# Kernel tuning notes

Hardware: AMD Instinct MI355X
Metric: run time of the kernel (lower is better)

The kernel has to match this reference:

```python
import jax, jax.numpy as jnp
import numpy as np

D_MODEL = 1024
D_FFN = 4096
NUM_EXPERTS = 8
TOP_K = 2
EPS = 1e-7


def setup_inputs() -> dict:
    key = jax.random.key(0)
    ks = jax.random.split(key, 10)
    B, T = 2, 2048
    s = 0.02
    return {
        "x": jax.random.normal(ks[0], (B, T, D_MODEL), dtype=jnp.float32),
        "padding_mask": jnp.ones((B, T), dtype=bool),
        "rms_w": jnp.ones((D_MODEL,), dtype=jnp.float32),
        "router_w": jax.random.normal(ks[1], (NUM_EXPERTS, D_MODEL), dtype=jnp.float32) * s,
        "router_b": jnp.zeros((NUM_EXPERTS,), dtype=jnp.float32),
        "W1": jax.random.normal(ks[2], (NUM_EXPERTS, D_MODEL, D_FFN), dtype=jnp.float32) * s,
        "b1": jnp.zeros((NUM_EXPERTS, D_FFN), dtype=jnp.float32),
        "W2": jax.random.normal(ks[3], (NUM_EXPERTS, D_FFN, D_MODEL), dtype=jnp.float32) * s,
        "b2": jnp.zeros((NUM_EXPERTS, D_MODEL), dtype=jnp.float32),
        "W3": jax.random.normal(ks[4], (NUM_EXPERTS, D_MODEL, D_FFN), dtype=jnp.float32) * s,
        "b3": jnp.zeros((NUM_EXPERTS, D_FFN), dtype=jnp.float32),
    }


def reference(x, padding_mask, rms_w, router_w, router_b, W1, b1, W2, b2, W3, b3):
    B, T, d = x.shape
    # RMSNorm
    rms = jnp.sqrt(jnp.mean(x * x, axis=-1, keepdims=True) + EPS)
    xn = rms_w * (x / rms)
    xf = xn.reshape(-1, d)  # [N, d]

    # Router: softmax -> top-k -> renormalize
    logits = xf @ router_w.T + router_b            # [N, E]
    probs = jax.nn.softmax(logits, axis=-1)
    topv, topi = jax.lax.top_k(probs, TOP_K)       # [N, K]
    w = topv / jnp.sum(topv, axis=-1, keepdims=True)
    # Dense combine weights per (token, expert): sum of top-k weights routed to e
    combine = jnp.sum(jax.nn.one_hot(topi, NUM_EXPERTS, dtype=xf.dtype) * w[..., None], axis=1)  # [N, E]

    # Loop over experts via scan (one full-token SwiGLU FFN per expert, masked combine)
    def step(acc, params):
        W1e, b1e, W2e, b2e, W3e, b3e, ce = params
        h = jax.nn.silu(xf @ W1e + b1e) * (xf @ W3e + b3e)  # [N, d_ffn]
        y = h @ W2e + b2e                                    # [N, d]
        return acc + ce[:, None] * y, None

    out, _ = jax.lax.scan(step, jnp.zeros_like(xf), (W1, b1, W2, b2, W3, b3, combine.T))
    aux_loss = jnp.asarray(0.0, dtype=x.dtype)  # use_aux_loss only active in training mode
    return out.reshape(B, T, d), aux_loss
```

## Files before the change

kernel.cpp:

```cpp
#include <hip/hip_runtime.h>
#include <stdint.h>


#define NTOK 4096
#define DM   1024
#define DF   4096
#define NE   8
#define BM   128
#define MAX_RB 72
#define SLOT_CAP (MAX_RB * BM)

typedef _Float16 f16;
typedef __attribute__((ext_vector_type(8))) _Float16 f16x8;
typedef __attribute__((ext_vector_type(4))) _Float16 f16x4;
typedef __attribute__((ext_vector_type(4))) float    f32x4;
typedef __attribute__((ext_vector_type(2))) float    f32x2;

__device__ __forceinline__ void gl2lds16(const void* g, void* l) {
  __builtin_amdgcn_global_load_lds(
      (const __attribute__((address_space(1))) unsigned int*)g,
      (__attribute__((address_space(3))) unsigned int*)l, 16, 0, 0);
}

__global__ __launch_bounds__(256) void k_rms_router(
    const float* __restrict__ x, const float* __restrict__ rms_w,
    const float* __restrict__ rw, const float* __restrict__ rbias,
    f16* __restrict__ xn, int* __restrict__ topi, float* __restrict__ topw,
    int* __restrict__ counts)
{
  int t = blockIdx.x;
  int tid = threadIdx.x;
  const float* xr = x + (size_t)t * DM;
  f32x4 xv = *(const f32x4*)(xr + tid * 4);
  f32x4 gw = *(const f32x4*)(rms_w + tid * 4);
  f32x4 gv = xv * gw;

  float v[9];
  v[8] = xv[0]*xv[0] + xv[1]*xv[1] + xv[2]*xv[2] + xv[3]*xv[3];
#pragma unroll
  for (int e = 0; e < NE; ++e) {
    f32x4 wv = *(const f32x4*)(rw + e * DM + tid * 4);
    v[e] = gv[0]*wv[0] + gv[1]*wv[1] + gv[2]*wv[2] + gv[3]*wv[3];
  }
#pragma unroll
  for (int off = 32; off; off >>= 1) {
#pragma unroll
    for (int j = 0; j < 9; ++j) v[j] += __shfl_xor(v[j], off);
  }
  __shared__ float red[4][9];
  int wave = tid >> 6, lane = tid & 63;
  if (lane == 0) {
#pragma unroll
    for (int j = 0; j < 9; ++j) red[wave][j] = v[j];
  }
  __syncthreads();
  float tot[9];
#pragma unroll
  for (int j = 0; j < 9; ++j)
    tot[j] = red[0][j] + red[1][j] + red[2][j] + red[3][j];

  float rinv = 1.0f / sqrtf(tot[8] * (1.0f / DM) + 1e-7f);
  float lg[NE];
#pragma unroll
  for (int e = 0; e < NE; ++e) lg[e] = tot[e] * rinv + rbias[e];

  int e1 = 0; float b1v = lg[0];
#pragma unroll
  for (int e = 1; e < NE; ++e) if (lg[e] > b1v) { b1v = lg[e]; e1 = e; }
  int e2 = -1; float b2v = -1e30f;
#pragma unroll
  for (int e = 0; e < NE; ++e) if (e != e1 && lg[e] > b2v) { b2v = lg[e]; e2 = e; }

  float r2 = expf(b2v - b1v);
  float w1 = 1.0f / (1.0f + r2);
  float w2 = r2 * w1;

  if (tid == 0) {
    topi[t * 2 + 0] = e1; topi[t * 2 + 1] = e2;
    topw[t * 2 + 0] = w1; topw[t * 2 + 1] = w2;
    atomicAdd(&counts[e1], 1);
    atomicAdd(&counts[e2], 1);
  }
  f16x4 o;
#pragma unroll
  for (int i = 0; i < 4; ++i) o[i] = (f16)(gv[i] * rinv);
  *(f16x4*)(xn + (size_t)t * DM + tid * 4) = o;
}

__global__ void k_build(const int* __restrict__ counts, int* __restrict__ po,
                        int2* __restrict__ rbtable, int* __restrict__ total_rb)
{
  if (threadIdx.x != 0 || blockIdx.x != 0) return;
  int off = 0, idx = 0;
  for (int e = 0; e < NE; ++e) {
    int c = counts[e];
    po[e] = off;
    int nrb = (c + BM - 1) / BM;
    for (int r = 0; r < nrb; ++r) { rbtable[idx] = make_int2(e, off + r * BM); ++idx; }
    off += nrb * BM;
  }
  *total_rb = idx;
}

__global__ __launch_bounds__(256) void k_assign(
    const int* __restrict__ topi, const float* __restrict__ topw,
    const int* __restrict__ po, int* __restrict__ cursors,
    int* __restrict__ slot_token, float* __restrict__ slot_w,
    int* __restrict__ tok2slot)
{
  int t = blockIdx.x * 256 + threadIdx.x;
  if (t >= NTOK) return;
#pragma unroll
  for (int k = 0; k < 2; ++k) {
    int e = topi[t * 2 + k];
    int pos = atomicAdd(&cursors[e], 1);
    int slot = po[e] + pos;
    slot_token[slot] = t;
    slot_w[slot] = topw[t * 2 + k];
    tok2slot[t * 2 + k] = slot;
  }
}

__global__ __launch_bounds__(256) void k_convw(
    const float* __restrict__ W1, const float* __restrict__ W3,
    f16* __restrict__ w16)
{
  __shared__ f16 T[64][132];
  int g = blockIdx.x;
  int tensor = g >> 12;
  int rem = g & 4095;
  int e = rem >> 9;
  int t = rem & 511;
  const float* W = (tensor == 0) ? W1 : W3;
  int np = t >> 4, kt = t & 15;
  const float* src = W + (size_t)e * DM * DF + (size_t)(kt * 64) * DF + np * 128;

  int tid = threadIdx.x;
  int q = tid & 31, kb = tid >> 5;
#pragma unroll
  for (int i = 0; i < 8; ++i) {
    int k = kb + 8 * i;
    f32x4 v = *(const f32x4*)(src + (size_t)k * DF + q * 4);
    f16x4 h4 = { (f16)v[0], (f16)v[1], (f16)v[2], (f16)v[3] };
    *(f16x4*)(&T[k][q * 4]) = h4;
  }
  __syncthreads();
  int n = tid >> 1;
  f16* dst = w16 + ((size_t)(tensor * NE + e) * 512 + t) * 8192 + n * 64 + (tid & 1) * 32;
#pragma unroll
  for (int qq = 0; qq < 4; ++qq) {
    int cs = (tid & 1) * 4 + qq;
    int cl = cs ^ (n & 7);
    f16x8 o;
#pragma unroll
    for (int j = 0; j < 8; ++j) o[j] = T[cl * 8 + j][n];
    *(f16x8*)(dst + qq * 8) = o;
  }
}

__global__ __launch_bounds__(256, 3) void k_ffn13(
    const f16* __restrict__ xn, const int* __restrict__ slot_token,
    const int2* __restrict__ rbtable, const int* __restrict__ total_rb,
    const f16* __restrict__ w16,
    const float* __restrict__ b1, const float* __restrict__ b3,
    const float* __restrict__ W2, f16* __restrict__ w16_w2,
    f16* __restrict__ h)
{
  __shared__ __align__(16) f16 As[128 * 64];
  __shared__ __align__(16) f16 Bs[2][128 * 64];

  int bid = blockIdx.x;
  int wl = (bid & 7) * 288 + (bid >> 3);
  int rbi = wl % 72;
  int np  = wl / 72;
  int tid = threadIdx.x, lane = tid & 63, wave = tid >> 6;

  bool active = (rbi < *total_rb);
  if (active) {
    int2 ent = rbtable[rbi];
    int e = ent.x, row0 = ent.y;
    int n0 = np * 128;

    int wm = wave >> 1, wn = wave & 1;
    const f16* wb1 = w16 + ((size_t)(0 * NE + e) * 512 + np * 16) * 8192;
    const f16* wb3 = w16 + ((size_t)(1 * NE + e) * 512 + np * 16) * 8192;

    int tok[4];
#pragma unroll
    for (int q = 0; q < 4; ++q) {
      int m = q * 32 + wave * 8 + (lane >> 3);
      int tkn = slot_token[row0 + m];
      tok[q] = (tkn < 0) ? 0 : tkn;
    }
    int csx = (((lane & 7) ^ (lane >> 3)) << 3);
    int lin = wave * 512 + lane * 8;

    f32x4 acc1[4][4], acc3[4][4];
    f32x4 z = {0.f, 0.f, 0.f, 0.f};
#pragma unroll
    for (int i = 0; i < 4; ++i)
#pragma unroll
      for (int j = 0; j < 4; ++j) { acc1[i][j] = z; acc3[i][j] = z; }

    for (int kt = 0; kt < DM / 64; ++kt) {
      int k0 = kt * 64;
      const f16* s1 = wb1 + (size_t)kt * 8192;
      const f16* s3 = wb3 + (size_t)kt * 8192;
#pragma unroll
      for (int q = 0; q < 4; ++q) {
        gl2lds16(xn + (size_t)tok[q] * DM + k0 + csx,
                 (char*)As + q * 4096 + wave * 1024);
        gl2lds16(s1 + q * 2048 + lin, (char*)Bs[0] + q * 4096 + wave * 1024);
        gl2lds16(s3 + q * 2048 + lin, (char*)Bs[1] + q * 4096 + wave * 1024);
      }
      __syncthreads();
#pragma unroll
      for (int kh = 0; kh < 2; ++kh) {
        int kk = kh * 32 + (lane >> 4) * 8;
        f16x8 a[4];
#pragma unroll
        for (int fm = 0; fm < 4; ++fm) {
          int m = wm * 64 + fm * 16 + (lane & 15);
          a[fm] = *(const f16x8*)((char*)As + m * 128 + 2 * (kk ^ ((m & 7) << 3)));
        }
#pragma unroll
        for (int fn = 0; fn < 4; ++fn) {
          int n = wn * 64 + fn * 16 + (lane & 15);
          f16x8 bf1 = *(const f16x8*)((char*)Bs[0] + n * 128 + 2 * (kk ^ ((n & 7) << 3)));
          f16x8 bf3 = *(const f16x8*)((char*)Bs[1] + n * 128 + 2 * (kk ^ ((n & 7) << 3)));
#pragma unroll
          for (int fm = 0; fm < 4; ++fm) {
            acc1[fm][fn] = __builtin_amdgcn_mfma_f32_16x16x32_f16(a[fm], bf1, acc1[fm][fn], 0, 0, 0);
            acc3[fm][fn] = __builtin_amdgcn_mfma_f32_16x16x32_f16(a[fm], bf3, acc3[fm][fn], 0, 0, 0);
          }
        }
      }
      __syncthreads();
    }
#pragma unroll
    for (int fn = 0; fn < 4; ++fn) {
      int nc = n0 + wn * 64 + fn * 16 + (lane & 15);
      float bb1 = b1[e * DF + nc], bb3 = b3[e * DF + nc];
#pragma unroll
      for (int fm = 0; fm < 4; ++fm) {
        int mbase = wm * 64 + fm * 16 + (lane >> 4) * 4;
#pragma unroll
        for (int r = 0; r < 4; ++r) {
          int sl = mbase + r;
          float u1 = acc1[fm][fn][r] + bb1;
          float u3 = acc3[fm][fn][r] + bb3;
          float hv = (u1 / (1.0f + __expf(-u1))) * u3;
          size_t off = (size_t)(row0 + sl) * DF + (nc & ~63)
                     + ((((nc >> 3) & 7) ^ (sl & 7)) << 3) + (nc & 7);
          h[off] = (f16)hv;
        }
      }
    }
  }

  f16 (*T)[132] = (f16(*)[132])(&Bs[0][0]);
  int q = tid & 31, kb = tid >> 5;
  for (int j = 0; j < 2; ++j) {
    int tile = bid * 2 + j;
    if (tile >= NE * 512) break;
    int e2 = tile >> 9, t2 = tile & 511;
    int np2 = t2 >> 6, kt2 = t2 & 63;
    const float* src = W2 + (size_t)e2 * DM * DF + (size_t)(kt2 * 64) * DM + np2 * 128;
    __syncthreads();
#pragma unroll
    for (int i = 0; i < 8; ++i) {
      int k = kb + 8 * i;
      f32x4 v = *(const f32x4*)(src + (size_t)k * DM + q * 4);
      f16x4 h4 = { (f16)v[0], (f16)v[1], (f16)v[2], (f16)v[3] };
      *(f16x4*)(&T[k][q * 4]) = h4;
    }
    __syncthreads();
    int n = tid >> 1;
    f16* dst = w16_w2 + (size_t)(e2 * 512 + t2) * 8192 + n * 64 + (tid & 1) * 32;
#pragma unroll
    for (int qq = 0; qq < 4; ++qq) {
      int cs = (tid & 1) * 4 + qq;
      int cl = cs ^ (n & 7);
      f16x8 o8;
#pragma unroll
      for (int jj = 0; jj < 8; ++jj) o8[jj] = T[cl * 8 + jj][n];
      *(f16x8*)(dst + qq * 8) = o8;
    }
  }
}

__global__ __launch_bounds__(256, 4) void k_ffn2(
    const f16* __restrict__ h,
    const int2* __restrict__ rbtable, const int* __restrict__ total_rb,
    const f16* __restrict__ w16_w2, f16* __restrict__ partial)
{
  int bid = blockIdx.x;
  int wl = (bid & 7) * 144 + (bid >> 3);
  int rbi = wl % 72;
  int rest = wl / 72;
  int kc = rest & 1;
  int np = rest >> 1;
  if (rbi >= *total_rb) return;
  int2 ent = rbtable[rbi];
  int e = ent.x, row0 = ent.y;
  int n0 = np * 128;

  __shared__ __align__(16) f16 As[128 * 64];
  __shared__ __align__(16) f16 Bsh[128 * 64];

  int tid = threadIdx.x, lane = tid & 63, wave = tid >> 6;
  int wm = wave >> 1, wn = wave & 1;
  const f16* wb = w16_w2 + ((size_t)e * 512 + np * 64 + kc * 32) * 8192;
  int lin = wave * 512 + lane * 8;

  f32x4 acc[4][4];
  f32x4 z = {0.f, 0.f, 0.f, 0.f};
#pragma unroll
  for (int i = 0; i < 4; ++i)
#pragma unroll
    for (int j = 0; j < 4; ++j) acc[i][j] = z;

  for (int kt = 0; kt < 32; ++kt) {
    const f16* sB = wb + (size_t)kt * 8192;
    int k0 = kc * 2048 + kt * 64;
#pragma unroll
    for (int q = 0; q < 4; ++q) {
      int m = q * 32 + wave * 8 + (lane >> 3);
      gl2lds16(h + (size_t)(row0 + m) * DF + k0 + ((lane & 7) << 3),
               (char*)As + q * 4096 + wave * 1024);
      gl2lds16(sB + q * 2048 + lin, (char*)Bsh + q * 4096 + wave * 1024);
    }
    __syncthreads();
#pragma unroll
    for (int kh = 0; kh < 2; ++kh) {
      int kk = kh * 32 + (lane >> 4) * 8;
      f16x8 a[4];
#pragma unroll
      for (int fm = 0; fm < 4; ++fm) {
        int m = wm * 64 + fm * 16 + (lane & 15);
        a[fm] = *(const f16x8*)((char*)As + m * 128 + 2 * (kk ^ ((m & 7) << 3)));
      }
#pragma unroll
      for (int fn = 0; fn < 4; ++fn) {
        int n = wn * 64 + fn * 16 + (lane & 15);
        f16x8 bf = *(const f16x8*)((char*)Bsh + n * 128 + 2 * (kk ^ ((n & 7) << 3)));
#pragma unroll
        for (int fm = 0; fm < 4; ++fm)
          acc[fm][fn] = __builtin_amdgcn_mfma_f32_16x16x32_f16(a[fm], bf, acc[fm][fn], 0, 0, 0);
      }
    }
    __syncthreads();
  }
#pragma unroll
  for (int fn = 0; fn < 4; ++fn) {
    int nc = n0 + wn * 64 + fn * 16 + (lane & 15);
#pragma unroll
    for (int fm = 0; fm < 4; ++fm) {
      int mbase = wm * 64 + fm * 16 + (lane >> 4) * 4;
#pragma unroll
      for (int r = 0; r < 4; ++r) {
        int slot = row0 + mbase + r;
        partial[((size_t)(kc * SLOT_CAP + slot) << 10) + nc] = (f16)acc[fm][fn][r];
      }
    }
  }
}

__global__ __launch_bounds__(256) void k_combine(
    const f16* __restrict__ partial, const int* __restrict__ tok2slot,
    const int* __restrict__ topi, const float* __restrict__ topw,
    const float* __restrict__ b2, float* __restrict__ out)
{
  int t = blockIdx.x;
  int nc = threadIdx.x * 4;
  int s1 = tok2slot[t * 2], s2 = tok2slot[t * 2 + 1];
  float c1 = topw[t * 2], c2 = topw[t * 2 + 1];
  int e1 = topi[t * 2], e2 = topi[t * 2 + 1];
  float y1[4] = {0.f, 0.f, 0.f, 0.f}, y2[4] = {0.f, 0.f, 0.f, 0.f};
#pragma unroll
  for (int kc = 0; kc < 2; ++kc) {
    f16x4 p1 = *(const f16x4*)(partial + (((size_t)(kc * SLOT_CAP + s1)) << 10) + nc);
    f16x4 p2 = *(const f16x4*)(partial + (((size_t)(kc * SLOT_CAP + s2)) << 10) + nc);
#pragma unroll
    for (int i = 0; i < 4; ++i) { y1[i] += (float)p1[i]; y2[i] += (float)p2[i]; }
  }
  f32x4 bb1 = *(const f32x4*)(b2 + e1 * DM + nc);
  f32x4 bb2 = *(const f32x4*)(b2 + e2 * DM + nc);
  f32x4 o;
#pragma unroll
  for (int i = 0; i < 4; ++i)
    o[i] = c1 * (y1[i] + bb1[i]) + c2 * (y2[i] + bb2[i]);
  *(f32x4*)(out + ((size_t)t << 10) + nc) = o;
}

extern "C" void kernel_launch(void* const* d_in, const int* in_sizes, int n_in,
                              void* d_out, int out_size, void* d_ws, size_t ws_size,
                              hipStream_t stream)
{
  const float* x     = (const float*)d_in[0];
  const float* rms_w = (const float*)d_in[2];
  const float* rw    = (const float*)d_in[3];
  const float* rbias = (const float*)d_in[4];
  const float* W1    = (const float*)d_in[5];
  const float* b1    = (const float*)d_in[6];
  const float* W2    = (const float*)d_in[7];
  const float* b2    = (const float*)d_in[8];
  const float* W3    = (const float*)d_in[9];
  const float* b3    = (const float*)d_in[10];
  float* out = (float*)d_out;

  char* ws = (char*)d_ws;
  size_t o = 0;
  f16* w16 = (f16*)(ws + o); o += (size_t)3 * NE * 512 * 8192 * 2;
  f16* h   = (f16*)(ws + o); o += (size_t)SLOT_CAP * DF * 2;
  f16* xn  = (f16*)(ws + o); o += (size_t)NTOK * DM * 2;
  int*   slot_token = (int*)(ws + o);   o += SLOT_CAP * 4;
  float* slot_w     = (float*)(ws + o); o += SLOT_CAP * 4;
  int*   topi       = (int*)(ws + o);   o += NTOK * 2 * 4;
  float* topw       = (float*)(ws + o); o += NTOK * 2 * 4;
  int*   tok2slot   = (int*)(ws + o);   o += NTOK * 2 * 4;
  int*   counts     = (int*)(ws + o);   o += 64;
  int*   cursors    = (int*)(ws + o);   o += 64;
  int*   po         = (int*)(ws + o);   o += 64;
  int*   total_rb   = (int*)(ws + o);   o += 64;
  int2*  rbtable    = (int2*)(ws + o);  o += MAX_RB * 8;
  (void)ws_size; (void)in_sizes; (void)n_in;

  f16* w16_w2 = w16 + (size_t)2 * NE * 512 * 8192;

  f16* partial = w16;

  hipMemsetAsync(d_out, 0, (size_t)out_size * 4, stream);
  hipMemsetAsync(counts, 0, 128, stream);
  hipMemsetAsync(slot_token, 0xFF, SLOT_CAP * 4, stream);

  k_convw<<<2 * NE * 512, 256, 0, stream>>>(W1, W3, w16);
  k_rms_router<<<NTOK, 256, 0, stream>>>(x, rms_w, rw, rbias, xn, topi, topw, counts);
  k_build<<<1, 64, 0, stream>>>(counts, po, rbtable, total_rb);
  k_assign<<<16, 256, 0, stream>>>(topi, topw, po, cursors, slot_token, slot_w, tok2slot);
  k_ffn13<<<8 * 288, 256, 0, stream>>>(xn, slot_token, rbtable, total_rb,
                                       w16, b1, b3, W2, w16_w2, h);
  k_ffn2<<<8 * 144, 256, 0, stream>>>(h, rbtable, total_rb, w16_w2, partial);
  k_combine<<<NTOK, 256, 0, stream>>>(partial, tok2slot, topi, topw, b2, out);
}
```

Before: 536.3 us.

## Triple-buffer FFN GEMMs with 512-thread blocks and async LDS prefetch

Both FFN GEMM kernels now run with 512-thread blocks over one 144KB LDS buffer. K-tiles are staged three deep with global_load_lds, and the loop waits on vmcnt with a raw barrier instead of a full __syncthreads, so loads overlap MFMA work. s_setprio raises wave priority around the MFMA bursts. In k_ffn13, half the waves compute the W1 GEMM and half the W3 GEMM, and the W3 results pass through LDS for the SwiGLU epilogue. k_ffn2 now covers 256 output columns per block with a 4-way K split, which doubles the partial buffers that the combine kernel reads. Only one block fits per CU, and the 4-way split adds partial-sum traffic.

After: 592.1 us. +10.4%, slower.

```diff
diff --git a/kernel.cpp b/kernel.cpp
--- a/kernel.cpp
+++ b/kernel.cpp
@@ -14,7 +14,6 @@
 typedef __attribute__((ext_vector_type(8))) _Float16 f16x8;
 typedef __attribute__((ext_vector_type(4))) _Float16 f16x4;
 typedef __attribute__((ext_vector_type(4))) float    f32x4;
-typedef __attribute__((ext_vector_type(2))) float    f32x2;
 
 __device__ __forceinline__ void gl2lds16(const void* g, void* l) {
   __builtin_amdgcn_global_load_lds(
@@ -158,7 +157,7 @@
   }
 }
 
-__global__ __launch_bounds__(256, 3) void k_ffn13(
+__global__ __launch_bounds__(512, 2) void k_ffn13(
     const f16* __restrict__ xn, const int* __restrict__ slot_token,
     const int2* __restrict__ rbtable, const int* __restrict__ total_rb,
     const f16* __restrict__ w16,
@@ -166,8 +165,7 @@
     const float* __restrict__ W2, f16* __restrict__ w16_w2,
     f16* __restrict__ h)
 {
-  __shared__ __align__(16) f16 As[128 * 64];
-  __shared__ __align__(16) f16 Bs[2][128 * 64];
+  __shared__ __align__(16) char LB[147456];
 
   int bid = blockIdx.x;
   int wl = (bid & 7) * 288 + (bid >> 3);
@@ -180,106 +178,135 @@
     int2 ent = rbtable[rbi];
     int e = ent.x, row0 = ent.y;
     int n0 = np * 128;
-
-    int wm = wave >> 1, wn = wave & 1;
+    int wm = wave >> 2, wt = (wave >> 1) & 1, wn = wave & 1;
+
     const f16* wb1 = w16 + ((size_t)(0 * NE + e) * 512 + np * 16) * 8192;
     const f16* wb3 = w16 + ((size_t)(1 * NE + e) * 512 + np * 16) * 8192;
 
-    int tok[4];
-#pragma unroll
-    for (int q = 0; q < 4; ++q) {
-      int m = q * 32 + wave * 8 + (lane >> 3);
+    int tok[2];
+#pragma unroll
+    for (int q = 0; q < 2; ++q) {
+      int m = q * 64 + wave * 8 + (lane >> 3);
       int tkn = slot_token[row0 + m];
       tok[q] = (tkn < 0) ? 0 : tkn;
     }
     int csx = (((lane & 7) ^ (lane >> 3)) << 3);
     int lin = wave * 512 + lane * 8;
 
-    f32x4 acc1[4][4], acc3[4][4];
+    f32x4 acc[4][4];
     f32x4 z = {0.f, 0.f, 0.f, 0.f};
 #pragma unroll
     for (int i = 0; i < 4; ++i)
 #pragma unroll
-      for (int j = 0; j < 4; ++j) { acc1[i][j] = z; acc3[i][j] = z; }
-
-    for (int kt = 0; kt < DM / 64; ++kt) {
-      int k0 = kt * 64;
+      for (int j = 0; j < 4; ++j) acc[i][j] = z;
+
+    auto STAGE = [&](int kt, int ro) {
       const f16* s1 = wb1 + (size_t)kt * 8192;
       const f16* s3 = wb3 + (size_t)kt * 8192;
-#pragma unroll
-      for (int q = 0; q < 4; ++q) {
-        gl2lds16(xn + (size_t)tok[q] * DM + k0 + csx,
-                 (char*)As + q * 4096 + wave * 1024);
-        gl2lds16(s1 + q * 2048 + lin, (char*)Bs[0] + q * 4096 + wave * 1024);
-        gl2lds16(s3 + q * 2048 + lin, (char*)Bs[1] + q * 4096 + wave * 1024);
-      }
-      __syncthreads();
+      int k0 = kt * 64;
+#pragma unroll
+      for (int q = 0; q < 2; ++q) {
+        int d = ro + q * 8192 + wave * 1024 + lane * 16;
+        gl2lds16(xn + (size_t)tok[q] * DM + k0 + csx, LB + d);
+        gl2lds16(s1 + q * 4096 + lin, LB + 16384 + d);
+        gl2lds16(s3 + q * 4096 + lin, LB + 32768 + d);
+      }
+    };
+
+    STAGE(0, 0);
+    STAGE(1, 49152);
+    asm volatile("s_waitcnt vmcnt(6)" ::: "memory");
+    __builtin_amdgcn_s_barrier();
+
+    int cur = 0, nxt = 49152, fut = 98304;
+    for (int t = 0; t < 16; ++t) {
+      if (t + 2 < 16) STAGE(t + 2, fut);
+      int bofs = cur + 16384 + wt * 16384;
 #pragma unroll
       for (int kh = 0; kh < 2; ++kh) {
         int kk = kh * 32 + (lane >> 4) * 8;
-        f16x8 a[4];
+        f16x8 a[4], b[4];
+#pragma unroll
+        for (int f = 0; f < 4; ++f) {
+          int m = wm * 64 + f * 16 + (lane & 15);
+          a[f] = *(const f16x8*)(LB + cur + m * 128 + 2 * (kk ^ ((m & 7) << 3)));
+          int n = wn * 64 + f * 16 + (lane & 15);
+          b[f] = *(const f16x8*)(LB + bofs + n * 128 + 2 * (kk ^ ((n & 7) << 3)));
+        }
+        __builtin_amdgcn_s_setprio(1);
+#pragma unroll
+        for (int fn = 0; fn < 4; ++fn)
+#pragma unroll
+          for (int fm = 0; fm < 4; ++fm)
+            acc[fm][fn] = __builtin_amdgcn_mfma_f32_16x16x32_f16(a[fm], b[fn], acc[fm][fn], 0, 0, 0);
+        __builtin_amdgcn_s_setprio(0);
+      }
+      if (t < 15) {
+        if (t < 14) asm volatile("s_waitcnt vmcnt(6)" ::: "memory");
+        else        asm volatile("s_waitcnt vmcnt(0)" ::: "memory");
+        __builtin_amdgcn_s_barrier();
+        int tmp = cur; cur = nxt; nxt = fut; fut = tmp;
+      }
+    }
+
+    __syncthreads();
+    if (wt == 1) {
+      float* ex = (float*)LB + (wm * 2 + wn) * 4096;
+#pragma unroll
+      for (int fm = 0; fm < 4; ++fm)
+#pragma unroll
+        for (int fn = 0; fn < 4; ++fn)
+#pragma unroll
+          for (int r = 0; r < 4; ++r)
+            ex[(fm * 16 + (lane >> 4) * 4 + r) * 64 + fn * 16 + (lane & 15)] = acc[fm][fn][r];
+    }
+    __syncthreads();
+    if (wt == 0) {
+      const float* ex = (const float*)LB + (wm * 2 + wn) * 4096;
+#pragma unroll
+      for (int fn = 0; fn < 4; ++fn) {
+        int nc = n0 + wn * 64 + fn * 16 + (lane & 15);
+        float bb1 = b1[e * DF + nc], bb3 = b3[e * DF + nc];
 #pragma unroll
         for (int fm = 0; fm < 4; ++fm) {
-          int m = wm * 64 + fm * 16 + (lane & 15);
-          a[fm] = *(const f16x8*)((char*)As + m * 128 + 2 * (kk ^ ((m & 7) << 3)));
-        }
-#pragma unroll
-        for (int fn = 0; fn < 4; ++fn) {
-          int n = wn * 64 + fn * 16 + (lane & 15);
-          f16x8 bf1 = *(const f16x8*)((char*)Bs[0] + n * 128 + 2 * (kk ^ ((n & 7) << 3)));
-          f16x8 bf3 = *(const f16x8*)((char*)Bs[1] + n * 128 + 2 * (kk ^ ((n & 7) << 3)));
-#pragma unroll
-          for (int fm = 0; fm < 4; ++fm) {
-            acc1[fm][fn] = __builtin_amdgcn_mfma_f32_16x16x32_f16(a[fm], bf1, acc1[fm][fn], 0, 0, 0);
-            acc3[fm][fn] = __builtin_amdgcn_mfma_f32_16x16x32_f16(a[fm], bf3, acc3[fm][fn], 0, 0, 0);
+          int mbase = wm * 64 + fm * 16 + (lane >> 4) * 4;
+#pragma unroll
+          for (int r = 0; r < 4; ++r) {
+            int sl = mbase + r;
+            float u1 = acc[fm][fn][r] + bb1;
+            float u3 = ex[(fm * 16 + (lane >> 4) * 4 + r) * 64 + fn * 16 + (lane & 15)] + bb3;
+            float hv = (u1 / (1.0f + __expf(-u1))) * u3;
+            size_t off = (size_t)(row0 + sl) * DF + (nc & ~63)
+                       + ((((nc >> 3) & 7) ^ (sl & 7)) << 3) + (nc & 7);
+            h[off] = (f16)hv;
           }
         }
       }
-      __syncthreads();
-    }
-#pragma unroll
-    for (int fn = 0; fn < 4; ++fn) {
-      int nc = n0 + wn * 64 + fn * 16 + (lane & 15);
-      float bb1 = b1[e * DF + nc], bb3 = b3[e * DF + nc];
-#pragma unroll
-      for (int fm = 0; fm < 4; ++fm) {
-        int mbase = wm * 64 + fm * 16 + (lane >> 4) * 4;
-#pragma unroll
-        for (int r = 0; r < 4; ++r) {
-          int sl = mbase + r;
-          float u1 = acc1[fm][fn][r] + bb1;
-          float u3 = acc3[fm][fn][r] + bb3;
-          float hv = (u1 / (1.0f + __expf(-u1))) * u3;
-          size_t off = (size_t)(row0 + sl) * DF + (nc & ~63)
-                     + ((((nc >> 3) & 7) ^ (sl & 7)) << 3) + (nc & 7);
-          h[off] = (f16)hv;
-        }
-      }
-    }
-  }
-
-  f16 (*T)[132] = (f16(*)[132])(&Bs[0][0]);
+    }
+  }
+
+  f16 (*T)[132] = (f16(*)[132])LB;
   int q = tid & 31, kb = tid >> 5;
   for (int j = 0; j < 2; ++j) {
-    int tile = bid * 2 + j;
+    int tile = bid + j * 2304;
     if (tile >= NE * 512) break;
     int e2 = tile >> 9, t2 = tile & 511;
     int np2 = t2 >> 6, kt2 = t2 & 63;
     const float* src = W2 + (size_t)e2 * DM * DF + (size_t)(kt2 * 64) * DM + np2 * 128;
     __syncthreads();
 #pragma unroll
-    for (int i = 0; i < 8; ++i) {
-      int k = kb + 8 * i;
+    for (int i = 0; i < 4; ++i) {
+      int k = kb + 16 * i;
       f32x4 v = *(const f32x4*)(src + (size_t)k * DM + q * 4);
       f16x4 h4 = { (f16)v[0], (f16)v[1], (f16)v[2], (f16)v[3] };
       *(f16x4*)(&T[k][q * 4]) = h4;
     }
     __syncthreads();
-    int n = tid >> 1;
-    f16* dst = w16_w2 + (size_t)(e2 * 512 + t2) * 8192 + n * 64 + (tid & 1) * 32;
-#pragma unroll
-    for (int qq = 0; qq < 4; ++qq) {
-      int cs = (tid & 1) * 4 + qq;
+    int n = tid >> 2, sub = tid & 3;
+    f16* dst = w16_w2 + (size_t)(e2 * 512 + t2) * 8192 + n * 64 + sub * 16;
+#pragma unroll
+    for (int qq = 0; qq < 2; ++qq) {
+      int cs = sub * 2 + qq;
       int cl = cs ^ (n & 7);
       f16x8 o8;
 #pragma unroll
@@ -289,29 +316,29 @@
   }
 }
 
-__global__ __launch_bounds__(256, 4) void k_ffn2(
+__global__ __launch_bounds__(512, 2) void k_ffn2(
     const f16* __restrict__ h,
     const int2* __restrict__ rbtable, const int* __restrict__ total_rb,
     const f16* __restrict__ w16_w2, f16* __restrict__ partial)
 {
+  __shared__ __align__(16) char LB[147456];
+
   int bid = blockIdx.x;
   int wl = (bid & 7) * 144 + (bid >> 3);
   int rbi = wl % 72;
   int rest = wl / 72;
-  int kc = rest & 1;
-  int np = rest >> 1;
+  int kc = rest & 3;
+  int npp = rest >> 2;
   if (rbi >= *total_rb) return;
   int2 ent = rbtable[rbi];
   int e = ent.x, row0 = ent.y;
-  int n0 = np * 128;
-
-  __shared__ __align__(16) f16 As[128 * 64];
-  __shared__ __align__(16) f16 Bsh[128 * 64];
 
   int tid = threadIdx.x, lane = tid & 63, wave = tid >> 6;
-  int wm = wave >> 1, wn = wave & 1;
-  const f16* wb = w16_w2 + ((size_t)e * 512 + np * 64 + kc * 32) * 8192;
+  int wm = wave >> 2, wn = wave & 3;
+  const f16* wp0 = w16_w2 + ((size_t)e * 512 + (npp * 2) * 64 + kc * 16) * 8192;
+  const f16* wp1 = wp0 + (size_t)64 * 8192;
   int lin = wave * 512 + lane * 8;
+  int arow = wave * 8 + (lane >> 3);
 
   f32x4 acc[4][4];
   f32x4 z = {0.f, 0.f, 0.f, 0.f};
@@ -320,40 +347,57 @@
 #pragma unroll
     for (int j = 0; j < 4; ++j) acc[i][j] = z;
 
-  for (int kt = 0; kt < 32; ++kt) {
-    const f16* sB = wb + (size_t)kt * 8192;
-    int k0 = kc * 2048 + kt * 64;
-#pragma unroll
-    for (int q = 0; q < 4; ++q) {
-      int m = q * 32 + wave * 8 + (lane >> 3);
-      gl2lds16(h + (size_t)(row0 + m) * DF + k0 + ((lane & 7) << 3),
-               (char*)As + q * 4096 + wave * 1024);
-      gl2lds16(sB + q * 2048 + lin, (char*)Bsh + q * 4096 + wave * 1024);
-    }
-    __syncthreads();
+  auto STAGE = [&](int kt, int ro) {
+    int k0 = kc * 1024 + kt * 64;
+#pragma unroll
+    for (int q = 0; q < 2; ++q) {
+      int d = ro + q * 8192 + wave * 1024 + lane * 16;
+      gl2lds16(h + (size_t)(row0 + q * 64 + arow) * DF + k0 + ((lane & 7) << 3), LB + d);
+      gl2lds16(wp0 + (size_t)kt * 8192 + q * 4096 + lin, LB + 16384 + d);
+      gl2lds16(wp1 + (size_t)kt * 8192 + q * 4096 + lin, LB + 32768 + d);
+    }
+  };
+
+  STAGE(0, 0);
+  STAGE(1, 49152);
+  asm volatile("s_waitcnt vmcnt(6)" ::: "memory");
+  __builtin_amdgcn_s_barrier();
+
+  int cur = 0, nxt = 49152, fut = 98304;
+  for (int t = 0; t < 16; ++t) {
+    if (t + 2 < 16) STAGE(t + 2, fut);
 #pragma unroll
     for (int kh = 0; kh < 2; ++kh) {
       int kk = kh * 32 + (lane >> 4) * 8;
-      f16x8 a[4];
-#pragma unroll
-      for (int fm = 0; fm < 4; ++fm) {
-        int m = wm * 64 + fm * 16 + (lane & 15);
-        a[fm] = *(const f16x8*)((char*)As + m * 128 + 2 * (kk ^ ((m & 7) << 3)));
-      }
-#pragma unroll
-      for (int fn = 0; fn < 4; ++fn) {
-        int n = wn * 64 + fn * 16 + (lane & 15);
-        f16x8 bf = *(const f16x8*)((char*)Bsh + n * 128 + 2 * (kk ^ ((n & 7) << 3)));
+      f16x8 a[4], b[4];
+#pragma unroll
+      for (int f = 0; f < 4; ++f) {
+        int m = wm * 64 + f * 16 + (lane & 15);
+        a[f] = *(const f16x8*)(LB + cur + m * 128 + 2 * (kk ^ ((m & 7) << 3)));
+        int n = wn * 64 + f * 16 + (lane & 15);
+        int pane = n >> 7, nn = n & 127;
+        b[f] = *(const f16x8*)(LB + cur + 16384 + pane * 16384
+                               + nn * 128 + 2 * (kk ^ ((nn & 7) << 3)));
+      }
+      __builtin_amdgcn_s_setprio(1);
+#pragma unroll
+      for (int fn = 0; fn < 4; ++fn)
 #pragma unroll
         for (int fm = 0; fm < 4; ++fm)
-          acc[fm][fn] = __builtin_amdgcn_mfma_f32_16x16x32_f16(a[fm], bf, acc[fm][fn], 0, 0, 0);
-      }
-    }
-    __syncthreads();
-  }
+          acc[fm][fn] = __builtin_amdgcn_mfma_f32_16x16x32_f16(a[fm], b[fn], acc[fm][fn], 0, 0, 0);
+      __builtin_amdgcn_s_setprio(0);
+    }
+    if (t < 15) {
+      if (t < 14) asm volatile("s_waitcnt vmcnt(6)" ::: "memory");
+      else        asm volatile("s_waitcnt vmcnt(0)" ::: "memory");
+      __builtin_amdgcn_s_barrier();
+      int tmp = cur; cur = nxt; nxt = fut; fut = tmp;
+    }
+  }
+
 #pragma unroll
   for (int fn = 0; fn < 4; ++fn) {
-    int nc = n0 + wn * 64 + fn * 16 + (lane & 15);
+    int nc = npp * 256 + wn * 64 + fn * 16 + (lane & 15);
 #pragma unroll
     for (int fm = 0; fm < 4; ++fm) {
       int mbase = wm * 64 + fm * 16 + (lane >> 4) * 4;
@@ -378,7 +422,7 @@
   int e1 = topi[t * 2], e2 = topi[t * 2 + 1];
   float y1[4] = {0.f, 0.f, 0.f, 0.f}, y2[4] = {0.f, 0.f, 0.f, 0.f};
 #pragma unroll
-  for (int kc = 0; kc < 2; ++kc) {
+  for (int kc = 0; kc < 4; ++kc) {
     f16x4 p1 = *(const f16x4*)(partial + (((size_t)(kc * SLOT_CAP + s1)) << 10) + nc);
     f16x4 p2 = *(const f16x4*)(partial + (((size_t)(kc * SLOT_CAP + s2)) << 10) + nc);
 #pragma unroll
@@ -427,7 +471,6 @@
   (void)ws_size; (void)in_sizes; (void)n_in;
 
   f16* w16_w2 = w16 + (size_t)2 * NE * 512 * 8192;
-
   f16* partial = w16;
 
   hipMemsetAsync(d_out, 0, (size_t)out_size * 4, stream);
@@ -438,8 +481,8 @@
   k_rms_router<<<NTOK, 256, 0, stream>>>(x, rms_w, rw, rbias, xn, topi, topw, counts);
   k_build<<<1, 64, 0, stream>>>(counts, po, rbtable, total_rb);
   k_assign<<<16, 256, 0, stream>>>(topi, topw, po, cursors, slot_token, slot_w, tok2slot);
-  k_ffn13<<<8 * 288, 256, 0, stream>>>(xn, slot_token, rbtable, total_rb,
+  k_ffn13<<<8 * 288, 512, 0, stream>>>(xn, slot_token, rbtable, total_rb,
                                        w16, b1, b3, W2, w16_w2, h);
-  k_ffn2<<<8 * 144, 256, 0, stream>>>(h, rbtable, total_rb, w16_w2, partial);
+  k_ffn2<<<8 * 144, 512, 0, stream>>>(h, rbtable, total_rb, w16_w2, partial);
   k_combine<<<NTOK, 256, 0, stream>>>(partial, tok2slot, topi, topw, b2, out);
 }
```

## Remap ffn block-to-XCD tiling and split ffn2 K into four chunks

Applied to the files above, without the earlier changes.

Changes the block-index mapping in k_ffn13 so each XCD handles a fixed range of N-tiles across groups of row blocks, aiming for better L2 reuse of weight tiles within an XCD. k_ffn2 now splits the K dimension into four chunks instead of two, doubling the grid and mapping row blocks to XCDs, which adds parallelism and shortens each block's K loop. The cost is twice as much f16 partial-sum traffic and more reads in k_combine. The four partial slabs must still fit in the reused w16 buffer.

Result: faster. 525.6 us (-2.0%).

```diff
diff --git a/kernel.cpp b/kernel.cpp
--- a/kernel.cpp
+++ b/kernel.cpp
@@ -14,7 +14,6 @@
 typedef __attribute__((ext_vector_type(8))) _Float16 f16x8;
 typedef __attribute__((ext_vector_type(4))) _Float16 f16x4;
 typedef __attribute__((ext_vector_type(4))) float    f32x4;
-typedef __attribute__((ext_vector_type(2))) float    f32x2;
 
 __device__ __forceinline__ void gl2lds16(const void* g, void* l) {
   __builtin_amdgcn_global_load_lds(
@@ -170,9 +169,9 @@
   __shared__ __align__(16) f16 Bs[2][128 * 64];
 
   int bid = blockIdx.x;
-  int wl = (bid & 7) * 288 + (bid >> 3);
-  int rbi = wl % 72;
-  int np  = wl / 72;
+  int xcd = bid & 7, i = bid >> 3;
+  int rbi = (i / 12) * 3 + (i % 3);
+  int np  = xcd * 4 + ((i / 3) & 3);
   int tid = threadIdx.x, lane = tid & 63, wave = tid >> 6;
 
   bool active = (rbi < *total_rb);
@@ -198,9 +197,9 @@
     f32x4 acc1[4][4], acc3[4][4];
     f32x4 z = {0.f, 0.f, 0.f, 0.f};
 #pragma unroll
-    for (int i = 0; i < 4; ++i)
-#pragma unroll
-      for (int j = 0; j < 4; ++j) { acc1[i][j] = z; acc3[i][j] = z; }
+    for (int i2 = 0; i2 < 4; ++i2)
+#pragma unroll
+      for (int j = 0; j < 4; ++j) { acc1[i2][j] = z; acc3[i2][j] = z; }
 
     for (int kt = 0; kt < DM / 64; ++kt) {
       int k0 = kt * 64;
@@ -268,8 +267,8 @@
     const float* src = W2 + (size_t)e2 * DM * DF + (size_t)(kt2 * 64) * DM + np2 * 128;
     __syncthreads();
 #pragma unroll
-    for (int i = 0; i < 8; ++i) {
-      int k = kb + 8 * i;
+    for (int i2 = 0; i2 < 8; ++i2) {
+      int k = kb + 8 * i2;
       f32x4 v = *(const f32x4*)(src + (size_t)k * DM + q * 4);
       f16x4 h4 = { (f16)v[0], (f16)v[1], (f16)v[2], (f16)v[3] };
       *(f16x4*)(&T[k][q * 4]) = h4;
@@ -295,11 +294,12 @@
     const f16* __restrict__ w16_w2, f16* __restrict__ partial)
 {
   int bid = blockIdx.x;
-  int wl = (bid & 7) * 144 + (bid >> 3);
-  int rbi = wl % 72;
-  int rest = wl / 72;
-  int kc = rest & 1;
-  int np = rest >> 1;
+  int xcd = bid & 7, i = bid >> 3;
+  int rbi_in  = i % 3;
+  int np      = (i / 3) & 7;
+  int kc      = (i / 24) & 3;
+  int rbi_out = i / 96;
+  int rbi = xcd + 8 * (rbi_out * 3 + rbi_in);
   if (rbi >= *total_rb) return;
   int2 ent = rbtable[rbi];
   int e = ent.x, row0 = ent.y;
@@ -310,19 +310,19 @@
 
   int tid = threadIdx.x, lane = tid & 63, wave = tid >> 6;
   int wm = wave >> 1, wn = wave & 1;
-  const f16* wb = w16_w2 + ((size_t)e * 512 + np * 64 + kc * 32) * 8192;
+  const f16* wb = w16_w2 + ((size_t)e * 512 + np * 64 + kc * 16) * 8192;
   int lin = wave * 512 + lane * 8;
 
   f32x4 acc[4][4];
   f32x4 z = {0.f, 0.f, 0.f, 0.f};
 #pragma unroll
-  for (int i = 0; i < 4; ++i)
-#pragma unroll
-    for (int j = 0; j < 4; ++j) acc[i][j] = z;
-
-  for (int kt = 0; kt < 32; ++kt) {
+  for (int i2 = 0; i2 < 4; ++i2)
+#pragma unroll
+    for (int j = 0; j < 4; ++j) acc[i2][j] = z;
+
+  for (int kt = 0; kt < 16; ++kt) {
     const f16* sB = wb + (size_t)kt * 8192;
-    int k0 = kc * 2048 + kt * 64;
+    int k0 = kc * 1024 + kt * 64;
 #pragma unroll
     for (int q = 0; q < 4; ++q) {
       int m = q * 32 + wave * 8 + (lane >> 3);
@@ -378,7 +378,7 @@
   int e1 = topi[t * 2], e2 = topi[t * 2 + 1];
   float y1[4] = {0.f, 0.f, 0.f, 0.f}, y2[4] = {0.f, 0.f, 0.f, 0.f};
 #pragma unroll
-  for (int kc = 0; kc < 2; ++kc) {
+  for (int kc = 0; kc < 4; ++kc) {
     f16x4 p1 = *(const f16x4*)(partial + (((size_t)(kc * SLOT_CAP + s1)) << 10) + nc);
     f16x4 p2 = *(const f16x4*)(partial + (((size_t)(kc * SLOT_CAP + s2)) << 10) + nc);
 #pragma unroll
@@ -427,7 +427,6 @@
   (void)ws_size; (void)in_sizes; (void)n_in;
 
   f16* w16_w2 = w16 + (size_t)2 * NE * 512 * 8192;
-
   f16* partial = w16;
 
   hipMemsetAsync(d_out, 0, (size_t)out_size * 4, stream);
@@ -440,6 +439,6 @@
   k_assign<<<16, 256, 0, stream>>>(topi, topw, po, cursors, slot_token, slot_w, tok2slot);
   k_ffn13<<<8 * 288, 256, 0, stream>>>(xn, slot_token, rbtable, total_rb,
                                        w16, b1, b3, W2, w16_w2, h);
-  k_ffn2<<<8 * 144, 256, 0, stream>>>(h, rbtable, total_rb, w16_w2, partial);
+  k_ffn2<<<8 * 288, 256, 0, stream>>>(h, rbtable, total_rb, w16_w2, partial);
   k_combine<<<NTOK, 256, 0, stream>>>(partial, tok2slot, topi, topw, b2, out);
 }
```
